# Performance work log

Hardware: AMD Instinct MI355X
Metric: run time of the kernel (lower is better)

Reference implementation:

```python
import jax, jax.numpy as jnp
import numpy as np

RES = 7          # POOLER_RESOLUTION
SR = 2           # POOLER_SAMPLING_RATIO
SCALES = (0.25, 0.125, 0.0625, 0.03125)
CANONICAL_SCALE = 224.0
CANONICAL_LEVEL = 4.0
K_MIN, K_MAX = 2.0, 5.0  # -log2(SCALES[0]), -log2(SCALES[-1])


def setup_inputs() -> dict:
    key = jax.random.key(0)
    ks = jax.random.split(key, 9)
    feat0 = jax.random.normal(ks[0], (2, 256, 200, 200), dtype=jnp.float32)
    feat1 = jax.random.normal(ks[1], (2, 256, 100, 100), dtype=jnp.float32)
    feat2 = jax.random.normal(ks[2], (2, 256, 50, 50), dtype=jnp.float32)
    feat3 = jax.random.normal(ks[3], (2, 256, 25, 25), dtype=jnp.float32)
    R = 512
    x1 = jax.random.uniform(ks[4], (R,)) * 600.0
    y1 = jax.random.uniform(ks[5], (R,)) * 600.0
    w = 16.0 + jax.random.uniform(ks[6], (R,)) * 500.0
    h = 16.0 + jax.random.uniform(ks[7], (R,)) * 500.0
    boxes = jnp.stack([x1, y1, x1 + w, y1 + h], axis=1).astype(jnp.float32)
    batch_idx = jax.random.randint(ks[8], (R,), 0, 2, dtype=jnp.int32)
    return {"feat0": feat0, "feat1": feat1, "feat2": feat2, "feat3": feat3,
            "boxes": boxes, "batch_idx": batch_idx}


def _map_levels(boxes):
    # LevelMapper: floor(k0 + log2(sqrt(area)/224 + eps)), clamp to [k_min,k_max], shift
    area = jnp.maximum(boxes[:, 2] - boxes[:, 0], 0.0) * jnp.maximum(boxes[:, 3] - boxes[:, 1], 0.0)
    s = jnp.sqrt(area)
    lvl = jnp.floor(CANONICAL_LEVEL + jnp.log2(s / CANONICAL_SCALE + 1e-6))
    return (jnp.clip(lvl, K_MIN, K_MAX) - K_MIN).astype(jnp.int32)


def _roi_align(feat, boxes, batch_idx, scale):
    # feat: [B,C,H,W]; boxes: [R,4] (x1,y1,x2,y2) in image coords; ROIAlign (aligned=False)
    H, W = feat.shape[2], feat.shape[3]
    x1 = boxes[:, 0] * scale
    y1 = boxes[:, 1] * scale
    x2 = boxes[:, 2] * scale
    y2 = boxes[:, 3] * scale
    roi_w = jnp.maximum(x2 - x1, 1.0)
    roi_h = jnp.maximum(y2 - y1, 1.0)
    bin_w = roi_w / RES
    bin_h = roi_h / RES
    # sample-point offsets within the roi, in bin units: [RES*SR]
    p = (jnp.arange(RES, dtype=jnp.float32)[:, None]
         + (jnp.arange(SR, dtype=jnp.float32)[None, :] + 0.5) / SR).reshape(-1)
    ys = y1[:, None] + p[None, :] * bin_h[:, None]   # [R,S]
    xs = x1[:, None] + p[None, :] * bin_w[:, None]   # [R,S]
    valid_y = (ys >= -1.0) & (ys <= float(H))
    valid_x = (xs >= -1.0) & (xs <= float(W))
    yc = jnp.clip(ys, 0.0, float(H - 1))
    xc = jnp.clip(xs, 0.0, float(W - 1))
    y0 = jnp.floor(yc).astype(jnp.int32)
    x0 = jnp.floor(xc).astype(jnp.int32)
    y1i = jnp.minimum(y0 + 1, H - 1)
    x1i = jnp.minimum(x0 + 1, W - 1)
    ly = yc - y0.astype(jnp.float32)
    lx = xc - x0.astype(jnp.float32)
    hy = 1.0 - ly
    hx = 1.0 - lx
    b = batch_idx[:, None, None]  # [R,1,1]

    def gather(yi, xi):
        # advanced indexing -> [R,S,S,C]
        return feat[b, :, yi[:, :, None], xi[:, None, :]]

    v = (gather(y0, x0) * (hy[:, :, None] * hx[:, None, :])[..., None]
         + gather(y0, x1i) * (hy[:, :, None] * lx[:, None, :])[..., None]
         + gather(y1i, x0) * (ly[:, :, None] * hx[:, None, :])[..., None]
         + gather(y1i, x1i) * (ly[:, :, None] * lx[:, None, :])[..., None])
    v = v * (valid_y[:, :, None] & valid_x[:, None, :])[..., None].astype(v.dtype)
    R = boxes.shape[0]
    C = feat.shape[1]
    v = v.reshape(R, RES, SR, RES, SR, C).mean(axis=(2, 4))  # [R,RES,RES,C]
    return jnp.transpose(v, (0, 3, 1, 2))  # [R,C,RES,RES]


def reference(feat0, feat1, feat2, feat3, boxes, batch_idx):
    feats = (feat0, feat1, feat2, feat3)
    levels = _map_levels(boxes)
    out = jnp.zeros((boxes.shape[0], feat0.shape[1], RES, RES), dtype=feat0.dtype)
    for lvl, (f, sc) in enumerate(zip(feats, SCALES)):
        pooled = _roi_align(f, boxes, batch_idx, sc)
        out = out + jnp.where((levels == lvl)[:, None, None, None], pooled, 0.0)
    return out
```

## Files before the change

### kernel.cpp

```cpp
#include <hip/hip_runtime.h>
#include <hip/hip_bf16.h>

#define RES 7
#define NCH 256

__device__ __forceinline__ unsigned short f32_to_bf16_rne(float f) {
    unsigned int u = __float_as_uint(f);
    u += 0x7fffu + ((u >> 16) & 1u);
    return (unsigned short)(u >> 16);
}

__global__ __launch_bounds__(256) void transpose_all_bf16(
    const float* __restrict__ f0, const float* __restrict__ f1,
    const float* __restrict__ f2, const float* __restrict__ f3,
    unsigned short* __restrict__ ws)
{
    __shared__ float tile[32][33];

    const int x = blockIdx.x;
    const int l = (x >= 1250) + (x >= 1563) + (x >= 1642);

    const int base = (l == 0) ? 0 : (l == 1) ? 1250 : (l == 2) ? 1563 : 1642;
    const int HW   = (l == 0) ? 40000 : (l == 1) ? 10000 : (l == 2) ? 2500 : 625;
    const float* __restrict__ src =
        (l == 0) ? f0 : (l == 1) ? f1 : (l == 2) ? f2 : f3;
    const size_t doff = (l == 0) ? 0u : (l == 1) ? 20480000u
                      : (l == 2) ? 25600000u : 26880000u;

    const int b   = blockIdx.z;
    const int hw0 = (x - base) * 32;
    const int c0  = blockIdx.y * 32;
    const int tx  = threadIdx.x;
    const int ty  = threadIdx.y;

    const float* __restrict__ s    = src + (size_t)b * NCH * HW;
    unsigned short* __restrict__ d = ws + doff + (size_t)b * HW * NCH;

    const int hw_r = hw0 + tx;
#pragma unroll
    for (int i = 0; i < 32; i += 8) {
        const int c = c0 + ty + i;
        if (hw_r < HW) tile[ty + i][tx] = s[(size_t)c * HW + hw_r];
    }
    __syncthreads();
    const int c_w = c0 + tx;
#pragma unroll
    for (int i = 0; i < 32; i += 8) {
        const int hw = hw0 + ty + i;
        if (hw < HW) d[(size_t)hw * NCH + c_w] = f32_to_bf16_rne(tile[tx][ty + i]);
    }
}

__global__ __launch_bounds__(512) void roi_gather_nhwc_bf16(
    const unsigned short* __restrict__ ws,
    const float* __restrict__ boxes, const int* __restrict__ bidx,
    float* __restrict__ out)
{
    __shared__ float lds[49 * 260];

    const int r   = blockIdx.x;
    const int t   = threadIdx.x;
    const int cq  = t & 63;
    const int grp = t >> 6;

    const float bx1 = boxes[r * 4 + 0];
    const float by1 = boxes[r * 4 + 1];
    const float bx2 = boxes[r * 4 + 2];
    const float by2 = boxes[r * 4 + 3];

    const float area = fmaxf(bx2 - bx1, 0.0f) * fmaxf(by2 - by1, 0.0f);
    const float s    = sqrtf(area);
    const float lvlf = floorf(4.0f + log2f(s / 224.0f + 1e-6f));
    const int   lvl  = (int)(fminf(fmaxf(lvlf, 2.0f), 5.0f)) - 2;

    float scale; int H; size_t off;
    if      (lvl == 0) { scale = 0.25f;    H = 200; off = 0u; }
    else if (lvl == 1) { scale = 0.125f;   H = 100; off = 20480000u; }
    else if (lvl == 2) { scale = 0.0625f;  H = 50;  off = 25600000u; }
    else               { scale = 0.03125f; H = 25;  off = 26880000u; }
    const int W = H;

    const int b = bidx[r];
    const unsigned short* __restrict__ feat = ws + off + (size_t)b * H * W * NCH;

    const float x1 = bx1 * scale;
    const float y1 = by1 * scale;
    const float roi_w = fmaxf(bx2 * scale - x1, 1.0f);
    const float roi_h = fmaxf(by2 * scale - y1, 1.0f);
    const float bw = roi_w * (1.0f / RES);
    const float bh = roi_h * (1.0f / RES);

    for (int bin = grp; bin < 49; bin += 8) {
        const int py = bin / 7;
        const int px = bin - py * 7;

        float acc0 = 0.0f, acc1 = 0.0f, acc2 = 0.0f, acc3 = 0.0f;
#pragma unroll
        for (int sy = 0; sy < 2; ++sy) {
            const float pyf = (float)py + ((float)sy + 0.5f) * 0.5f;
            const float ysmp = y1 + pyf * bh;
            const bool  vy   = (ysmp >= -1.0f) && (ysmp <= (float)H);
            const float ycl  = fminf(fmaxf(ysmp, 0.0f), (float)(H - 1));
            const int   y0   = (int)floorf(ycl);
            const int   y1i  = min(y0 + 1, H - 1);
            const float ly   = ycl - (float)y0;
            const float hy   = 1.0f - ly;
#pragma unroll
            for (int sx = 0; sx < 2; ++sx) {
                const float pxf = (float)px + ((float)sx + 0.5f) * 0.5f;
                const float xsmp = x1 + pxf * bw;
                const bool  vx   = (xsmp >= -1.0f) && (xsmp <= (float)W);
                const float xcl  = fminf(fmaxf(xsmp, 0.0f), (float)(W - 1));
                const int   x0   = (int)floorf(xcl);
                const int   x1i  = min(x0 + 1, W - 1);
                const float lx   = xcl - (float)x0;
                const float hx   = 1.0f - lx;

                const float m   = (vy && vx) ? 1.0f : 0.0f;
                const float w00 = m * hy * hx;
                const float w01 = m * hy * lx;
                const float w10 = m * ly * hx;
                const float w11 = m * ly * lx;

                const uint2 u00 = *(const uint2*)(feat + ((size_t)(y0  * W + x0 )) * NCH + 4 * cq);
                const uint2 u01 = *(const uint2*)(feat + ((size_t)(y0  * W + x1i)) * NCH + 4 * cq);
                const uint2 u10 = *(const uint2*)(feat + ((size_t)(y1i * W + x0 )) * NCH + 4 * cq);
                const uint2 u11 = *(const uint2*)(feat + ((size_t)(y1i * W + x1i)) * NCH + 4 * cq);

                acc0 += w00 * __uint_as_float(u00.x << 16)
                      + w01 * __uint_as_float(u01.x << 16)
                      + w10 * __uint_as_float(u10.x << 16)
                      + w11 * __uint_as_float(u11.x << 16);
                acc1 += w00 * __uint_as_float(u00.x & 0xffff0000u)
                      + w01 * __uint_as_float(u01.x & 0xffff0000u)
                      + w10 * __uint_as_float(u10.x & 0xffff0000u)
                      + w11 * __uint_as_float(u11.x & 0xffff0000u);
                acc2 += w00 * __uint_as_float(u00.y << 16)
                      + w01 * __uint_as_float(u01.y << 16)
                      + w10 * __uint_as_float(u10.y << 16)
                      + w11 * __uint_as_float(u11.y << 16);
                acc3 += w00 * __uint_as_float(u00.y & 0xffff0000u)
                      + w01 * __uint_as_float(u01.y & 0xffff0000u)
                      + w10 * __uint_as_float(u10.y & 0xffff0000u)
                      + w11 * __uint_as_float(u11.y & 0xffff0000u);
            }
        }
        float4* dst = (float4*)&lds[bin * 260 + 4 * cq];
        *dst = make_float4(acc0 * 0.25f, acc1 * 0.25f, acc2 * 0.25f, acc3 * 0.25f);
    }

    __syncthreads();

    float* __restrict__ o = out + (size_t)r * (NCH * 49);
    for (int i = t; i < NCH * 49; i += 512) {
        const int ch = i / 49;
        const int bn = i - ch * 49;
        o[i] = lds[bn * 260 + ch];
    }
}

__global__ __launch_bounds__(256) void roi_align_fpn_kernel(
    const float* __restrict__ f0, const float* __restrict__ f1,
    const float* __restrict__ f2, const float* __restrict__ f3,
    const float* __restrict__ boxes, const int* __restrict__ bidx,
    float* __restrict__ out)
{
    const int r   = blockIdx.x;
    const int bin = blockIdx.y;
    const int c   = threadIdx.x;
    const int py  = bin / RES;
    const int px  = bin - py * RES;

    const float bx1 = boxes[r * 4 + 0];
    const float by1 = boxes[r * 4 + 1];
    const float bx2 = boxes[r * 4 + 2];
    const float by2 = boxes[r * 4 + 3];

    const float area = fmaxf(bx2 - bx1, 0.0f) * fmaxf(by2 - by1, 0.0f);
    const float s    = sqrtf(area);
    const float lvlf = floorf(4.0f + log2f(s / 224.0f + 1e-6f));
    const int   lvl  = (int)(fminf(fmaxf(lvlf, 2.0f), 5.0f)) - 2;

    const float scales[4] = {0.25f, 0.125f, 0.0625f, 0.03125f};
    const int   Hs[4]     = {200, 100, 50, 25};
    const float* feats[4] = {f0, f1, f2, f3};

    const float scale = scales[lvl];
    const int   H     = Hs[lvl];
    const int   W     = H;
    const float* feat = feats[lvl];

    const int b = bidx[r];

    const float x1 = bx1 * scale;
    const float y1 = by1 * scale;
    const float roi_w = fmaxf(bx2 * scale - x1, 1.0f);
    const float roi_h = fmaxf(by2 * scale - y1, 1.0f);
    const float bw = roi_w * (1.0f / RES);
    const float bh = roi_h * (1.0f / RES);

    const float* __restrict__ fc = feat + (size_t)(b * NCH + c) * H * W;

    float acc = 0.0f;
#pragma unroll
    for (int sy = 0; sy < 2; ++sy) {
        const float pyf = (float)py + ((float)sy + 0.5f) * 0.5f;
        const float ys  = y1 + pyf * bh;
        const bool  vy  = (ys >= -1.0f) && (ys <= (float)H);
        const float ycl = fminf(fmaxf(ys, 0.0f), (float)(H - 1));
        const int   y0  = (int)floorf(ycl);
        const int   y1i = min(y0 + 1, H - 1);
        const float ly  = ycl - (float)y0;
        const float hy  = 1.0f - ly;
#pragma unroll
        for (int sx = 0; sx < 2; ++sx) {
            const float pxf = (float)px + ((float)sx + 0.5f) * 0.5f;
            const float xs  = x1 + pxf * bw;
            const bool  vx  = (xs >= -1.0f) && (xs <= (float)W);
            const float xcl = fminf(fmaxf(xs, 0.0f), (float)(W - 1));
            const int   x0  = (int)floorf(xcl);
            const int   x1i = min(x0 + 1, W - 1);
            const float lx  = xcl - (float)x0;
            const float hx  = 1.0f - lx;

            const float v00 = fc[y0  * W + x0 ];
            const float v01 = fc[y0  * W + x1i];
            const float v10 = fc[y1i * W + x0 ];
            const float v11 = fc[y1i * W + x1i];

            const float v = v00 * (hy * hx) + v01 * (hy * lx)
                          + v10 * (ly * hx) + v11 * (ly * lx);
            if (vy && vx) acc += v;
        }
    }

    out[((size_t)r * NCH + c) * (RES * RES) + bin] = acc * 0.25f;
}

extern "C" void kernel_launch(void* const* d_in, const int* in_sizes, int n_in,
                              void* d_out, int out_size, void* d_ws, size_t ws_size,
                              hipStream_t stream)
{
    const float* f0    = (const float*)d_in[0];
    const float* f1    = (const float*)d_in[1];
    const float* f2    = (const float*)d_in[2];
    const float* f3    = (const float*)d_in[3];
    const float* boxes = (const float*)d_in[4];
    const int*   bidx  = (const int*)d_in[5];
    float* out = (float*)d_out;

    const int R = in_sizes[4] / 4;

    const size_t need = 27200000ull * sizeof(unsigned short);

    if (ws_size >= need) {
        unsigned short* ws = (unsigned short*)d_ws;
        dim3 tgrid(1662, 8, 2);
        dim3 tblock(32, 8);
        transpose_all_bf16<<<tgrid, tblock, 0, stream>>>(f0, f1, f2, f3, ws);
        roi_gather_nhwc_bf16<<<dim3(R), dim3(512), 0, stream>>>(ws, boxes, bidx, out);
    } else {
        dim3 grid(R, RES * RES);
        roi_align_fpn_kernel<<<grid, dim3(NCH), 0, stream>>>(f0, f1, f2, f3, boxes, bidx, out);
    }
}
```

Before: 53.35 us.

## Rewrite NCHW-to-NHWC bf16 transpose with float4 loads, full-channel tiles and 8-byte stores

The transpose kernel now gives each block 64 spatial positions across all 256 channels. It reads with float4 vector loads, converts to bf16 before staging in a padded LDS tile, and writes each row with 8-byte stores. Block IDs are remapped with an XCD-style interleave that spreads work across chiplets. The goal is to cut load and store instruction count and widen memory transactions on the bandwidth-bound preprocessing pass. The risks are LDS bank conflicts from the scattered 2-byte LDS writes and lower occupancy from the larger tile.

New measurement: 51.01 us. 4.4% less time.

```diff
diff --git a/kernel.cpp b/kernel.cpp
--- a/kernel.cpp
+++ b/kernel.cpp
@@ -10,44 +10,67 @@
     return (unsigned short)(u >> 16);
 }
 
-__global__ __launch_bounds__(256) void transpose_all_bf16(
+__global__ __launch_bounds__(512) void transpose_all_bf16_v2(
     const float* __restrict__ f0, const float* __restrict__ f1,
     const float* __restrict__ f2, const float* __restrict__ f3,
     unsigned short* __restrict__ ws)
 {
-    __shared__ float tile[32][33];
-
-    const int x = blockIdx.x;
-    const int l = (x >= 1250) + (x >= 1563) + (x >= 1642);
-
-    const int base = (l == 0) ? 0 : (l == 1) ? 1250 : (l == 2) ? 1563 : 1642;
+    __shared__ unsigned short lds[64 * 260];
+
+    int id = blockIdx.x;
+    id = (id & 7) * 208 + (id >> 3);
+
+    const int b = (id >= 832) ? 1 : 0;
+    const int x = b ? (id - 832) : id;
+
+    const int l = (x >= 625) + (x >= 782) + (x >= 822);
+    const int base = (l == 0) ? 0 : (l == 1) ? 625 : (l == 2) ? 782 : 822;
     const int HW   = (l == 0) ? 40000 : (l == 1) ? 10000 : (l == 2) ? 2500 : 625;
     const float* __restrict__ src =
         (l == 0) ? f0 : (l == 1) ? f1 : (l == 2) ? f2 : f3;
     const size_t doff = (l == 0) ? 0u : (l == 1) ? 20480000u
                       : (l == 2) ? 25600000u : 26880000u;
 
-    const int b   = blockIdx.z;
-    const int hw0 = (x - base) * 32;
-    const int c0  = blockIdx.y * 32;
-    const int tx  = threadIdx.x;
-    const int ty  = threadIdx.y;
-
+    const int hw0 = (x - base) * 64;
     const float* __restrict__ s    = src + (size_t)b * NCH * HW;
     unsigned short* __restrict__ d = ws + doff + (size_t)b * HW * NCH;
 
-    const int hw_r = hw0 + tx;
-#pragma unroll
-    for (int i = 0; i < 32; i += 8) {
-        const int c = c0 + ty + i;
-        if (hw_r < HW) tile[ty + i][tx] = s[(size_t)c * HW + hw_r];
+    const int t  = threadIdx.x;
+    const int hq = t & 15;
+    const int cr = t >> 4;
+    const int hwq = hw0 + 4 * hq;
+
+#pragma unroll
+    for (int g = 0; g < 8; ++g) {
+        const int c = cr + 32 * g;
+        unsigned short v0, v1, v2, v3;
+        if (hwq + 3 < HW) {
+            const float4 f = *(const float4*)(s + (size_t)c * HW + hwq);
+            v0 = f32_to_bf16_rne(f.x); v1 = f32_to_bf16_rne(f.y);
+            v2 = f32_to_bf16_rne(f.z); v3 = f32_to_bf16_rne(f.w);
+        } else {
+            v0 = (hwq + 0 < HW) ? f32_to_bf16_rne(s[(size_t)c * HW + hwq + 0]) : 0;
+            v1 = (hwq + 1 < HW) ? f32_to_bf16_rne(s[(size_t)c * HW + hwq + 1]) : 0;
+            v2 = (hwq + 2 < HW) ? f32_to_bf16_rne(s[(size_t)c * HW + hwq + 2]) : 0;
+            v3 = (hwq + 3 < HW) ? f32_to_bf16_rne(s[(size_t)c * HW + hwq + 3]) : 0;
+        }
+        lds[(4 * hq + 0) * 260 + c] = v0;
+        lds[(4 * hq + 1) * 260 + c] = v1;
+        lds[(4 * hq + 2) * 260 + c] = v2;
+        lds[(4 * hq + 3) * 260 + c] = v3;
     }
     __syncthreads();
-    const int c_w = c0 + tx;
-#pragma unroll
-    for (int i = 0; i < 32; i += 8) {
-        const int hw = hw0 + ty + i;
-        if (hw < HW) d[(size_t)hw * NCH + c_w] = f32_to_bf16_rne(tile[tx][ty + i]);
+
+    const int w  = t >> 6;
+    const int ln = t & 63;
+#pragma unroll
+    for (int j = 0; j < 8; ++j) {
+        const int hwl = w + 8 * j;
+        const int hw  = hw0 + hwl;
+        if (hw < HW) {
+            const uint2 p = *(const uint2*)&lds[hwl * 260 + 4 * ln];
+            *(uint2*)(d + (size_t)hw * NCH + 4 * ln) = p;
+        }
     }
 }
 
@@ -255,9 +278,7 @@
 
     if (ws_size >= need) {
         unsigned short* ws = (unsigned short*)d_ws;
-        dim3 tgrid(1662, 8, 2);
-        dim3 tblock(32, 8);
-        transpose_all_bf16<<<tgrid, tblock, 0, stream>>>(f0, f1, f2, f3, ws);
+        transpose_all_bf16_v2<<<dim3(1664), dim3(512), 0, stream>>>(f0, f1, f2, f3, ws);
         roi_gather_nhwc_bf16<<<dim3(R), dim3(512), 0, stream>>>(ws, boxes, bidx, out);
     } else {
         dim3 grid(R, RES * RES);
```
